# Kernel optimization log

Hardware: AMD Instinct MI355X
Metric: run time of the kernel (lower is better)

Reference implementation:

```python
import jax, jax.numpy as jnp
import numpy as np

B, H, L, DK, DV = 4, 16, 1024, 64, 64

def setup_inputs() -> dict:
    key = jax.random.key(0)
    k1, k2, k3, k4 = jax.random.split(key, 4)
    Q = jax.random.normal(k1, (B, H, L, DK), dtype=jnp.float32)
    K = jax.random.normal(k2, (B, H, L, DK), dtype=jnp.float32)
    V = jax.random.normal(k3, (B, H, L, DV), dtype=jnp.float32)
    attn_mask = jax.random.randint(k4, (B, H, L, L), 0, 2).astype(jnp.bool_)
    return {"Q": Q, "K": K, "V": V, "attn_mask": attn_mask}

def reference(Q, K, V, attn_mask):
    # NOTE: original torch code uses d_k = Q.size(1) == n_heads (a bug kept for fidelity)
    scale = 1.0 / jnp.sqrt(jnp.asarray(Q.shape[1], dtype=Q.dtype))
    scores = jnp.einsum('bhqd,bhkd->bhqk', Q, K) * scale
    scores = jnp.where(attn_mask, jnp.asarray(-1e9, dtype=scores.dtype), scores)
    attn = jax.nn.softmax(scores, axis=-1)
    context = jnp.einsum('bhqk,bhkv->bhqv', attn, V)
    return (context, attn)
```

## Files before the change

### kernel.cpp

```cpp
#include <hip/hip_runtime.h>
#include <hip/hip_bf16.h>

typedef _Float16 half8 __attribute__((ext_vector_type(8)));
typedef _Float16 half4 __attribute__((ext_vector_type(4)));
typedef _Float16 half2v __attribute__((ext_vector_type(2)));
typedef __fp16 fp16x2 __attribute__((ext_vector_type(2)));
typedef float f32x4 __attribute__((ext_vector_type(4)));
typedef int i32x4 __attribute__((ext_vector_type(4)));

#define BH_ 64
#define L_ 1024
#define DK_ 64

__device__ __forceinline__ unsigned short f2h(float f) {
    _Float16 h = (_Float16)f;
    return __builtin_bit_cast(unsigned short, h);
}
__device__ __forceinline__ unsigned int pk2h(float a, float b) {
    fp16x2 h = __builtin_amdgcn_cvt_pkrtz(a, b);
    return __builtin_bit_cast(unsigned int, h);
}

__global__ void prep_kv(const float* __restrict__ K, const float* __restrict__ V,
                        unsigned short* __restrict__ Kh, unsigned short* __restrict__ Vt) {
    __shared__ float lds[64][65];
    if (blockIdx.x < 4096) {
        int idx = blockIdx.x * 256 + threadIdx.x;
        float4 v = reinterpret_cast<const float4*>(K)[idx];
        ushort4 o;
        o.x = f2h(v.x); o.y = f2h(v.y); o.z = f2h(v.z); o.w = f2h(v.w);
        reinterpret_cast<ushort4*>(Kh)[idx] = o;
        return;
    }
    int b = blockIdx.x - 4096;
    int bh = b >> 4, kt = b & 15;
    int t = threadIdx.x;
    const float* Vb = V + ((size_t)bh * L_ + kt * 64) * DK_;
#pragma unroll
    for (int it = 0; it < 4; ++it) {
        int idx = it * 256 + t;
        int row = idx >> 4, c4 = idx & 15;
        float4 v = reinterpret_cast<const float4*>(Vb + (size_t)row * DK_)[c4];
        lds[row][c4 * 4 + 0] = v.x; lds[row][c4 * 4 + 1] = v.y;
        lds[row][c4 * 4 + 2] = v.z; lds[row][c4 * 4 + 3] = v.w;
    }
    __syncthreads();
    unsigned short* Vtb = Vt + (size_t)bh * 64 * L_ + kt * 64;
#pragma unroll
    for (int it = 0; it < 4; ++it) {
        int idx = it * 256 + t;
        int n = idx >> 4, c4 = idx & 15;
        ushort4 o;
        o.x = f2h(lds[c4 * 4 + 0][n]);
        o.y = f2h(lds[c4 * 4 + 1][n]);
        o.z = f2h(lds[c4 * 4 + 2][n]);
        o.w = f2h(lds[c4 * 4 + 3][n]);
        *reinterpret_cast<ushort4*>(Vtb + (size_t)n * L_ + c4 * 4) = o;
    }
}

__global__ __launch_bounds__(256, 4) void attn_main(
    const float* __restrict__ Q, const int* __restrict__ mask,
    const unsigned short* __restrict__ Kh, const unsigned short* __restrict__ Vt,
    float* __restrict__ ctx_out, float* __restrict__ attn_out)
{
    const int qt = blockIdx.x, bh = blockIdx.y;
    const int tid = threadIdx.x;
    const int w = tid >> 6;
    const int lane = tid & 63;
    const int lg = lane >> 4, lr = lane & 15;
    const int q0 = qt * 16;

    __shared__ float red[2][4][16];
    __shared__ union {
        unsigned short p[16][1024];
        float ctxbuf[4][16][68];
    } u;

    auto paddr = [&](int row, int col) -> unsigned short* {
        unsigned byte = (unsigned)row * 2048u +
                        (((unsigned)col * 2u) ^ (((unsigned)(row & 7)) << 4));
        return (unsigned short*)((char*)&u.p[0][0] + byte);
    };

    half8 qh[2];
    {
        const float* qp = Q + ((size_t)bh * L_ + q0 + lr) * DK_ + lg * 8;
#pragma unroll
        for (int f = 0; f < 2; ++f) {
            float4 a = *reinterpret_cast<const float4*>(qp + f * 32);
            float4 b = *reinterpret_cast<const float4*>(qp + f * 32 + 4);
            qh[f][0] = (_Float16)a.x; qh[f][1] = (_Float16)a.y;
            qh[f][2] = (_Float16)a.z; qh[f][3] = (_Float16)a.w;
            qh[f][4] = (_Float16)b.x; qh[f][5] = (_Float16)b.y;
            qh[f][6] = (_Float16)b.z; qh[f][7] = (_Float16)b.w;
        }
    }

    const size_t rowbase = ((size_t)bh * L_ + q0 + lr) * L_;
    const unsigned short* kp = Kh + ((size_t)bh * L_ + w * 256 + lr) * DK_ + lg * 8;
    const int* mp = mask + rowbase + w * 256 + lg * 4;

    unsigned int sh[16][2];
    float mx = -INFINITY;

    half8 kc0 = *reinterpret_cast<const half8*>(kp);
    half8 kc1 = *reinterpret_cast<const half8*>(kp + 32);

#pragma unroll
    for (int tt = 0; tt < 16; ++tt) {
        half8 kn0 = kc0, kn1 = kc1;
        if (tt < 15) {
            kn0 = *reinterpret_cast<const half8*>(kp + (tt + 1) * 1024);
            kn1 = *reinterpret_cast<const half8*>(kp + (tt + 1) * 1024 + 32);
        }
        f32x4 acc = {0.f, 0.f, 0.f, 0.f};
        acc = __builtin_amdgcn_mfma_f32_16x16x32_f16(kc0, qh[0], acc, 0, 0, 0);
        acc = __builtin_amdgcn_mfma_f32_16x16x32_f16(kc1, qh[1], acc, 0, 0, 0);
        float s0 = 0.25f * acc[0];
        float s1 = 0.25f * acc[1];
        float s2 = 0.25f * acc[2];
        float s3 = 0.25f * acc[3];
        sh[tt][0] = pk2h(s0, s1);
        sh[tt][1] = pk2h(s2, s3);
        mx = fmaxf(mx, fmaxf(fmaxf(s0, s1), fmaxf(s2, s3)));
        kc0 = kn0; kc1 = kn1;
    }

    i32x4 mreg0[8];
#pragma unroll
    for (int tt = 0; tt < 8; ++tt)
        mreg0[tt] = *reinterpret_cast<const i32x4*>(mp + tt * 16);

    mx = fmaxf(mx, __shfl_xor(mx, 16));
    mx = fmaxf(mx, __shfl_xor(mx, 32));
    if (lane < 16) red[0][w][lr] = mx;
    __syncthreads();
    const float gm = fmaxf(fmaxf(red[0][0][lr], red[0][1][lr]),
                           fmaxf(red[0][2][lr], red[0][3][lr]));

    i32x4 mreg1[8];
#pragma unroll
    for (int tt = 0; tt < 8; ++tt)
        mreg1[tt] = *reinterpret_cast<const i32x4*>(mp + (tt + 8) * 16);

    float lsum = 0.f;
#pragma unroll
    for (int tt = 0; tt < 16; ++tt) {
        half2v a = __builtin_bit_cast(half2v, sh[tt][0]);
        half2v b = __builtin_bit_cast(half2v, sh[tt][1]);
        i32x4 m = (tt < 8) ? mreg0[tt] : mreg1[tt - 8];
        float p0 = m[0] ? 0.f : __expf((float)a[0] - gm);
        float p1 = m[1] ? 0.f : __expf((float)a[1] - gm);
        float p2 = m[2] ? 0.f : __expf((float)b[0] - gm);
        float p3 = m[3] ? 0.f : __expf((float)b[1] - gm);
        lsum += (p0 + p1) + (p2 + p3);
        sh[tt][0] = pk2h(p0, p1);
        sh[tt][1] = pk2h(p2, p3);
    }
    lsum += __shfl_xor(lsum, 16);
    lsum += __shfl_xor(lsum, 32);
    if (lane < 16) red[1][w][lr] = lsum;

#pragma unroll
    for (int tt = 0; tt < 16; ++tt) {
        uint2 pr; pr.x = sh[tt][0]; pr.y = sh[tt][1];
        *reinterpret_cast<uint2*>(paddr(lr, w * 256 + tt * 16 + lg * 4)) = pr;
    }

    const unsigned short* vp = Vt + ((size_t)bh * 64 + lr) * L_ + w * 256 + lg * 8;
    f32x4 cacc[4] = {{0,0,0,0},{0,0,0,0},{0,0,0,0},{0,0,0,0}};
    half8 vb0 = *reinterpret_cast<const half8*>(vp);
    half8 vb1 = *reinterpret_cast<const half8*>(vp + 16384);
    half8 vb2 = *reinterpret_cast<const half8*>(vp + 32768);
    half8 vb3 = *reinterpret_cast<const half8*>(vp + 49152);

#pragma unroll
    for (int c = 0; c < 8; ++c) {
        half8 vn0 = vb0, vn1 = vb1, vn2 = vb2, vn3 = vb3;
        if (c < 7) {
            vn0 = *reinterpret_cast<const half8*>(vp + (c + 1) * 32);
            vn1 = *reinterpret_cast<const half8*>(vp + 16384 + (c + 1) * 32);
            vn2 = *reinterpret_cast<const half8*>(vp + 32768 + (c + 1) * 32);
            vn3 = *reinterpret_cast<const half8*>(vp + 49152 + (c + 1) * 32);
        }
        half8 pa = *reinterpret_cast<const half8*>(paddr(lr, w * 256 + c * 32 + lg * 8));
        cacc[0] = __builtin_amdgcn_mfma_f32_16x16x32_f16(pa, vb0, cacc[0], 0, 0, 0);
        cacc[1] = __builtin_amdgcn_mfma_f32_16x16x32_f16(pa, vb1, cacc[1], 0, 0, 0);
        cacc[2] = __builtin_amdgcn_mfma_f32_16x16x32_f16(pa, vb2, cacc[2], 0, 0, 0);
        cacc[3] = __builtin_amdgcn_mfma_f32_16x16x32_f16(pa, vb3, cacc[3], 0, 0, 0);
        vb0 = vn0; vb1 = vn1; vb2 = vn2; vb3 = vn3;
    }

    __syncthreads();

    half4 preg[4][4];
    float rqv[4];
#pragma unroll
    for (int rr = 0; rr < 4; ++rr) {
        const int q = w * 4 + rr;
        rqv[rr] = 1.0f / (red[1][0][q] + red[1][1][q] +
                          red[1][2][q] + red[1][3][q]);
#pragma unroll
        for (int i = 0; i < 4; ++i)
            preg[rr][i] = *reinterpret_cast<const half4*>(paddr(q, i * 256 + lane * 4));
    }

    __syncthreads();

#pragma unroll
    for (int nt = 0; nt < 4; ++nt)
#pragma unroll
        for (int r = 0; r < 4; ++r)
            u.ctxbuf[w][lg * 4 + r][nt * 16 + lr] = cacc[nt][r];
    __syncthreads();
    {
        int e = tid * 4;
        int q = e >> 6, n = e & 63;
        float gs = red[1][0][q] + red[1][1][q] + red[1][2][q] + red[1][3][q];
        float rq = 1.0f / gs;
        float4 a0 = *reinterpret_cast<float4*>(&u.ctxbuf[0][q][n]);
        float4 a1 = *reinterpret_cast<float4*>(&u.ctxbuf[1][q][n]);
        float4 a2 = *reinterpret_cast<float4*>(&u.ctxbuf[2][q][n]);
        float4 a3 = *reinterpret_cast<float4*>(&u.ctxbuf[3][q][n]);
        float4 o;
        o.x = (a0.x + a1.x + a2.x + a3.x) * rq;
        o.y = (a0.y + a1.y + a2.y + a3.y) * rq;
        o.z = (a0.z + a1.z + a2.z + a3.z) * rq;
        o.w = (a0.w + a1.w + a2.w + a3.w) * rq;
        *reinterpret_cast<float4*>(&ctx_out[((size_t)bh * L_ + q0 + q) * DK_ + n]) = o;
    }

#pragma unroll
    for (int rr = 0; rr < 4; ++rr) {
        const int q = w * 4 + rr;
        const float rq = rqv[rr];
        float* orow = attn_out + ((size_t)bh * L_ + q0 + q) * L_;
#pragma unroll
        for (int i = 0; i < 4; ++i) {
            half4 v = preg[rr][i];
            float4 o;
            o.x = (float)v[0] * rq; o.y = (float)v[1] * rq;
            o.z = (float)v[2] * rq; o.w = (float)v[3] * rq;
            *reinterpret_cast<float4*>(orow + i * 256 + lane * 4) = o;
        }
    }
}

extern "C" void kernel_launch(void* const* d_in, const int* in_sizes, int n_in,
                              void* d_out, int out_size, void* d_ws, size_t ws_size,
                              hipStream_t stream) {
    const float* Q = (const float*)d_in[0];
    const float* K = (const float*)d_in[1];
    const float* V = (const float*)d_in[2];
    const int* mask = (const int*)d_in[3];
    float* ctx_out = (float*)d_out;
    float* attn_out = ctx_out + (size_t)BH_ * L_ * DK_;

    unsigned short* Kh = (unsigned short*)d_ws;
    unsigned short* Vt = Kh + (size_t)BH_ * L_ * DK_;

    hipLaunchKernelGGL(prep_kv, dim3(5120), dim3(256), 0, stream, K, V, Kh, Vt);
    hipLaunchKernelGGL(attn_main, dim3(64, 64), dim3(256), 0, stream,
                       Q, mask, Kh, Vt, ctx_out, attn_out);
}
```

Measured before the change: 215.1 us.

## Split mask loading by tile parity and use nontemporal stores for outputs

Even query tiles now load their mask rows up front with coalesced int4 reads and compress them into 4-bit nibbles in LDS, which are read during softmax. Odd tiles instead read the mask on demand inside the softmax loop rather than prefetching it into registers. Both ctx and attn outputs are written with nontemporal stores to reduce cache pollution from the large attn write. The aim is to stagger mask traffic across blocks and cut register pressure, at the cost of extra LDS use and divergent code paths per block.

```diff
diff --git a/kernel.cpp b/kernel.cpp
--- a/kernel.cpp
+++ b/kernel.cpp
@@ -19,6 +19,10 @@
 __device__ __forceinline__ unsigned int pk2h(float a, float b) {
     fp16x2 h = __builtin_amdgcn_cvt_pkrtz(a, b);
     return __builtin_bit_cast(unsigned int, h);
+}
+__device__ __forceinline__ void nt_store4(float* p, float a, float b, float c, float d) {
+    f32x4 v = {a, b, c, d};
+    __builtin_nontemporal_store(v, reinterpret_cast<f32x4*>(p));
 }
 
 __global__ void prep_kv(const float* __restrict__ K, const float* __restrict__ V,
@@ -70,7 +74,9 @@
     const int lane = tid & 63;
     const int lg = lane >> 4, lr = lane & 15;
     const int q0 = qt * 16;
-
+    const bool early = (qt & 1) == 0;
+
+    __shared__ unsigned char mnib[16][272];
     __shared__ float red[2][4][16];
     __shared__ union {
         unsigned short p[16][1024];
@@ -82,6 +88,23 @@
                         (((unsigned)col * 2u) ^ (((unsigned)(row & 7)) << 4));
         return (unsigned short*)((char*)&u.p[0][0] + byte);
     };
+
+    if (early) {
+#pragma unroll
+        for (int rr = 0; rr < 4; ++rr) {
+            const int row = w * 4 + rr;
+            const int* mrow = mask + ((size_t)bh * L_ + q0 + row) * L_;
+#pragma unroll
+            for (int j = 0; j < 4; ++j) {
+                int4 v = *reinterpret_cast<const int4*>(mrow + j * 256 + lane * 4);
+                unsigned nib = unsigned(v.x != 0)
+                             | (unsigned(v.y != 0) << 1)
+                             | (unsigned(v.z != 0) << 2)
+                             | (unsigned(v.w != 0) << 3);
+                mnib[row][j * 64 + lane] = (unsigned char)nib;
+            }
+        }
+    }
 
     half8 qh[2];
     {
@@ -127,11 +150,6 @@
         kc0 = kn0; kc1 = kn1;
     }
 
-    i32x4 mreg0[8];
-#pragma unroll
-    for (int tt = 0; tt < 8; ++tt)
-        mreg0[tt] = *reinterpret_cast<const i32x4*>(mp + tt * 16);
-
     mx = fmaxf(mx, __shfl_xor(mx, 16));
     mx = fmaxf(mx, __shfl_xor(mx, 32));
     if (lane < 16) red[0][w][lr] = mx;
@@ -139,24 +157,37 @@
     const float gm = fmaxf(fmaxf(red[0][0][lr], red[0][1][lr]),
                            fmaxf(red[0][2][lr], red[0][3][lr]));
 
-    i32x4 mreg1[8];
-#pragma unroll
-    for (int tt = 0; tt < 8; ++tt)
-        mreg1[tt] = *reinterpret_cast<const i32x4*>(mp + (tt + 8) * 16);
-
     float lsum = 0.f;
-#pragma unroll
-    for (int tt = 0; tt < 16; ++tt) {
-        half2v a = __builtin_bit_cast(half2v, sh[tt][0]);
-        half2v b = __builtin_bit_cast(half2v, sh[tt][1]);
-        i32x4 m = (tt < 8) ? mreg0[tt] : mreg1[tt - 8];
-        float p0 = m[0] ? 0.f : __expf((float)a[0] - gm);
-        float p1 = m[1] ? 0.f : __expf((float)a[1] - gm);
-        float p2 = m[2] ? 0.f : __expf((float)b[0] - gm);
-        float p3 = m[3] ? 0.f : __expf((float)b[1] - gm);
-        lsum += (p0 + p1) + (p2 + p3);
-        sh[tt][0] = pk2h(p0, p1);
-        sh[tt][1] = pk2h(p2, p3);
+    if (early) {
+        const unsigned char* mn = &mnib[lr][w * 64];
+#pragma unroll
+        for (int tt = 0; tt < 16; ++tt) {
+            half2v a = __builtin_bit_cast(half2v, sh[tt][0]);
+            half2v b = __builtin_bit_cast(half2v, sh[tt][1]);
+            unsigned nv = *reinterpret_cast<const unsigned int*>(&mn[tt * 4]);
+            unsigned nib = (nv >> (lg * 8)) & 0xFu;
+            float p0 = (nib & 1u) ? 0.f : __expf((float)a[0] - gm);
+            float p1 = (nib & 2u) ? 0.f : __expf((float)a[1] - gm);
+            float p2 = (nib & 4u) ? 0.f : __expf((float)b[0] - gm);
+            float p3 = (nib & 8u) ? 0.f : __expf((float)b[1] - gm);
+            lsum += (p0 + p1) + (p2 + p3);
+            sh[tt][0] = pk2h(p0, p1);
+            sh[tt][1] = pk2h(p2, p3);
+        }
+    } else {
+#pragma unroll
+        for (int tt = 0; tt < 16; ++tt) {
+            half2v a = __builtin_bit_cast(half2v, sh[tt][0]);
+            half2v b = __builtin_bit_cast(half2v, sh[tt][1]);
+            i32x4 m = *reinterpret_cast<const i32x4*>(mp + tt * 16);
+            float p0 = m[0] ? 0.f : __expf((float)a[0] - gm);
+            float p1 = m[1] ? 0.f : __expf((float)a[1] - gm);
+            float p2 = m[2] ? 0.f : __expf((float)b[0] - gm);
+            float p3 = m[3] ? 0.f : __expf((float)b[1] - gm);
+            lsum += (p0 + p1) + (p2 + p3);
+            sh[tt][0] = pk2h(p0, p1);
+            sh[tt][1] = pk2h(p2, p3);
+        }
     }
     lsum += __shfl_xor(lsum, 16);
     lsum += __shfl_xor(lsum, 32);
@@ -223,12 +254,11 @@
         float4 a1 = *reinterpret_cast<float4*>(&u.ctxbuf[1][q][n]);
         float4 a2 = *reinterpret_cast<float4*>(&u.ctxbuf[2][q][n]);
         float4 a3 = *reinterpret_cast<float4*>(&u.ctxbuf[3][q][n]);
-        float4 o;
-        o.x = (a0.x + a1.x + a2.x + a3.x) * rq;
-        o.y = (a0.y + a1.y + a2.y + a3.y) * rq;
-        o.z = (a0.z + a1.z + a2.z + a3.z) * rq;
-        o.w = (a0.w + a1.w + a2.w + a3.w) * rq;
-        *reinterpret_cast<float4*>(&ctx_out[((size_t)bh * L_ + q0 + q) * DK_ + n]) = o;
+        nt_store4(&ctx_out[((size_t)bh * L_ + q0 + q) * DK_ + n],
+                  (a0.x + a1.x + a2.x + a3.x) * rq,
+                  (a0.y + a1.y + a2.y + a3.y) * rq,
+                  (a0.z + a1.z + a2.z + a3.z) * rq,
+                  (a0.w + a1.w + a2.w + a3.w) * rq);
     }
 
 #pragma unroll
@@ -239,10 +269,9 @@
 #pragma unroll
         for (int i = 0; i < 4; ++i) {
             half4 v = preg[rr][i];
-            float4 o;
-            o.x = (float)v[0] * rq; o.y = (float)v[1] * rq;
-            o.z = (float)v[2] * rq; o.w = (float)v[3] * rq;
-            *reinterpret_cast<float4*>(orow + i * 256 + lane * 4) = o;
+            nt_store4(orow + i * 256 + lane * 4,
+                      (float)v[0] * rq, (float)v[1] * rq,
+                      (float)v[2] * rq, (float)v[3] * rq);
         }
     }
 }
```

New measurement: 222.3 us. +3.3%, slower.
